# Optimization experiments

Hardware: AMD Instinct MI355X
Metric: run time of the kernel (lower is better)

Reference implementation:

```python
import jax, jax.numpy as jnp
import numpy as np

N, E, D, H, Z, HEADS = 20000, 160000, 3000, 512, 50, 3
EPS = 1e-5


def _bn(x, gamma, beta):
    # BatchNorm1d, training-mode stats (biased variance), eps=1e-5
    m = x.mean(axis=0)
    v = x.var(axis=0)
    return (x - m) * jax.lax.rsqrt(v + EPS) * gamma + beta


def _gat(x, src, dst, n, W, att_src, att_dst, bias, heads, c):
    # PyG GATConv, concat=False (mean over heads), negative_slope=0.2
    h = (x @ W).reshape(n, heads, c)                      # [N,H,C]
    a_s = (h * att_src).sum(-1)                           # [N,H]
    a_d = (h * att_dst).sum(-1)                           # [N,H]
    e = jax.nn.leaky_relu(a_s[src] + a_d[dst], 0.2)       # [Etot,H]
    e = e - jax.ops.segment_max(e, dst, num_segments=n)[dst]
    ex = jnp.exp(e)
    den = jax.ops.segment_sum(ex, dst, num_segments=n)[dst]
    alpha = ex / den                                      # segment softmax over incoming edges
    msg = h[src] * alpha[:, :, None]                      # [Etot,H,C]
    out = jax.ops.segment_sum(msg, dst, num_segments=n)   # [N,H,C]
    return out.mean(axis=1) + bias


def setup_inputs() -> dict:
    key = jax.random.key(0)
    ks = jax.random.split(key, 16)
    s = 0.05
    inp = {
        "x": jax.random.normal(ks[0], (N, D), dtype=jnp.float32),
        "edge_index": jax.random.randint(ks[1], (2, E), 0, N, dtype=jnp.int64),
        "W1": jax.random.normal(ks[2], (D, HEADS * H), dtype=jnp.float32) * s,
        "att_src1": jax.random.normal(ks[3], (HEADS, H), dtype=jnp.float32) * s,
        "att_dst1": jax.random.normal(ks[4], (HEADS, H), dtype=jnp.float32) * s,
        "b1": jnp.zeros((H,), jnp.float32),
        "bn1_g": jnp.ones((H,), jnp.float32),
        "bn1_b": jnp.zeros((H,), jnp.float32),
        "W2": jax.random.normal(ks[5], (H, HEADS * Z), dtype=jnp.float32) * s,
        "att_src2": jax.random.normal(ks[6], (HEADS, Z), dtype=jnp.float32) * s,
        "att_dst2": jax.random.normal(ks[7], (HEADS, Z), dtype=jnp.float32) * s,
        "b2": jnp.zeros((Z,), jnp.float32),
        "bn2_g": jnp.ones((Z,), jnp.float32),
        "bn2_b": jnp.zeros((Z,), jnp.float32),
        "lin1_w": jax.random.normal(ks[8], (H, Z), dtype=jnp.float32) * s,
        "lin1_b": jnp.zeros((H,), jnp.float32),
        "dbn_g": jnp.ones((H,), jnp.float32),
        "dbn_b": jnp.zeros((H,), jnp.float32),
        "lin2_w": jax.random.normal(ks[9], (D, H), dtype=jnp.float32) * s,
        "lin2_b": jnp.zeros((D,), jnp.float32),
    }
    return inp


def reference(x, edge_index, W1, att_src1, att_dst1, b1, bn1_g, bn1_b,
              W2, att_src2, att_dst2, b2, bn2_g, bn2_b,
              lin1_w, lin1_b, dbn_g, dbn_b, lin2_w, lin2_b):
    n = x.shape[0]
    loop = jnp.arange(n, dtype=edge_index.dtype)
    src = jnp.concatenate([edge_index[0], loop])  # add self-loops (PyG default)
    dst = jnp.concatenate([edge_index[1], loop])
    h = jax.nn.relu(_bn(_gat(x, src, dst, n, W1, att_src1, att_dst1, b1, HEADS, H), bn1_g, bn1_b))
    z = jax.nn.relu(_bn(_gat(h, src, dst, n, W2, att_src2, att_dst2, b2, HEADS, Z), bn2_g, bn2_b))
    d = jax.nn.relu(_bn(z @ lin1_w.T + lin1_b, dbn_g, dbn_b))
    out = jax.nn.relu(d @ lin2_w.T + lin2_b)
    return out
```

## Files before the change

### kernel.cpp

```cpp
#include <hip/hip_runtime.h>
#include <stdint.h>

typedef unsigned short u16;
typedef __attribute__((ext_vector_type(8))) short s16x8;
typedef __attribute__((ext_vector_type(4))) short s16x4;
typedef __attribute__((ext_vector_type(4))) float f32x4;

#define DEVFN static __device__ __forceinline__

static constexpr int NN = 20000;
static constexpr int EE = 160000;
static constexpr int ET = 180000;
static constexpr int DD = 3000;
static constexpr int HH = 512;
static constexpr int ZZ = 50;
static constexpr int C1 = 1536;
static constexpr int C2 = 150;
static constexpr int KA1 = 3008;
static constexpr int KP1 = 3072;

DEVFN u16 f2b(float f) {
  uint32_t u = __builtin_bit_cast(uint32_t, f);
  u += 0x7FFFu + ((u >> 16) & 1u);
  return (u16)(u >> 16);
}
DEVFN float b2f(u16 b) {
  uint32_t u = ((uint32_t)b) << 16;
  return __builtin_bit_cast(float, u);
}
DEVFN int edge_at(const void* ei, int mode32, long idx) {
  return mode32 ? ((const int*)ei)[idx] : (int)((const long long*)ei)[idx];
}

typedef __attribute__((address_space(1))) const unsigned int gas_uint;
typedef __attribute__((address_space(3))) unsigned int las_uint;
DEVFN void async16(const u16* g, u16* l) {
  __builtin_amdgcn_global_load_lds((gas_uint*)(uintptr_t)g,
                                   (las_uint*)(unsigned)(uintptr_t)l, 16, 0, 0);
}

__global__ void k_detect(const int* __restrict__ ei, int* __restrict__ mode) {
  __shared__ int nz;
  if (threadIdx.x == 0) nz = 0;
  __syncthreads();
  int loc = 0;
  for (int i = threadIdx.x; i < 1024; i += blockDim.x)
    if (ei[2 * i + 1] != 0) loc = 1;
  if (loc) atomicOr(&nz, 1);
  __syncthreads();
  if (threadIdx.x == 0) *mode = nz;
}

__global__ void k_deg(const void* ei, const int* __restrict__ mode, int* __restrict__ deg) {
  int m = *mode;
  long i = (long)blockIdx.x * blockDim.x + threadIdx.x;
  long st = (long)gridDim.x * blockDim.x;
  for (; i < ET; i += st) {
    int d = (i < EE) ? edge_at(ei, m, EE + i) : (int)(i - EE);
    if ((unsigned)d < (unsigned)NN) atomicAdd(&deg[d], 1);
  }
}

__global__ void k_scan_blk(const int* __restrict__ deg, int* __restrict__ rowptr,
                           int* __restrict__ bsum) {
  __shared__ int buf[256];
  int b = blockIdx.x, tid = threadIdx.x;
  int i = b * 256 + tid;
  buf[tid] = (i < NN) ? deg[i] : 0;
  __syncthreads();
  for (int off = 1; off < 256; off <<= 1) {
    int t = (tid >= off) ? buf[tid - off] : 0;
    __syncthreads();
    buf[tid] += t;
    __syncthreads();
  }
  if (i < NN) rowptr[i + 1] = buf[tid];
  if (tid == 255) bsum[b] = buf[255];
}
__global__ void k_scan_top(int* __restrict__ bsum, int nb) {
  __shared__ int buf[128];
  int tid = threadIdx.x;
  buf[tid] = (tid < nb) ? bsum[tid] : 0;
  __syncthreads();
  for (int off = 1; off < 128; off <<= 1) {
    int t = (tid >= off) ? buf[tid - off] : 0;
    __syncthreads();
    buf[tid] += t;
    __syncthreads();
  }
  if (tid < nb) bsum[tid] = buf[tid];
}
__global__ void k_scan_add(int* __restrict__ rowptr, const int* __restrict__ bsum) {
  int b = blockIdx.x, tid = threadIdx.x;
  int i = b * 256 + tid;
  if (i == 0) rowptr[0] = 0;
  if (b > 0 && i < NN) rowptr[i + 1] += bsum[b - 1];
}

__global__ void k_fill(const void* ei, const int* __restrict__ mode,
                       const int* __restrict__ rowptr, int* __restrict__ cursor,
                       int* __restrict__ srcp) {
  int m = *mode;
  long i = (long)blockIdx.x * blockDim.x + threadIdx.x;
  long st = (long)gridDim.x * blockDim.x;
  for (; i < ET; i += st) {
    int s, d;
    if (i < EE) { s = edge_at(ei, m, i); d = edge_at(ei, m, EE + i); }
    else { s = d = (int)(i - EE); }
    if ((unsigned)d < (unsigned)NN && (unsigned)s < (unsigned)NN) {
      int pos = atomicAdd(&cursor[d], 1);
      srcp[rowptr[d] + pos] = s;
    }
  }
}

__global__ void k_cvt_pad4(const float* __restrict__ in, u16* __restrict__ out,
                           int R, int Cin, int ldo) {
  int r = blockIdx.y;
  int c = (blockIdx.x * blockDim.x + threadIdx.x) * 4;
  if (c >= ldo) return;
  s16x4 o;
  const float* src = in + (size_t)r * Cin + c;
  if (r < R && c + 4 <= Cin && ((((size_t)r * Cin + c) & 3) == 0)) {
    f32x4 v = *(const f32x4*)src;
#pragma unroll
    for (int j = 0; j < 4; j++) o[j] = (short)f2b(v[j]);
  } else {
#pragma unroll
    for (int j = 0; j < 4; j++)
      o[j] = (short)((r < R && c + j < Cin) ? f2b(src[j]) : (u16)0);
  }
  *(s16x4*)(out + (size_t)r * ldo + c) = o;
}

__global__ void k_transpose_tile(const float* __restrict__ in, u16* __restrict__ out,
                                 int R, int Cc, int ldo) {
  __shared__ float t[32][33];
  int tx = threadIdx.x & 31, ty = threadIdx.x >> 5;
  int c0 = blockIdx.x * 32, r0 = blockIdx.y * 32;
#pragma unroll
  for (int j = 0; j < 4; j++) {
    int r = r0 + ty + j * 8, c = c0 + tx;
    t[ty + j * 8][tx] = (r < R && c < Cc) ? in[(size_t)r * Cc + c] : 0.f;
  }
  __syncthreads();
#pragma unroll
  for (int j = 0; j < 4; j++) {
    int c = c0 + ty + j * 8, r = r0 + tx;
    if (c < Cc && r < ldo) out[(size_t)c * ldo + r] = f2b(t[tx][ty + j * 8]);
  }
}

__global__ void k_transpose_cvt2(const float* __restrict__ in, u16* __restrict__ out,
                                 int R, int C, int Cp, int ldo) {
  long total = (long)Cp * ldo;
  long i = (long)blockIdx.x * blockDim.x + threadIdx.x;
  long st = (long)gridDim.x * blockDim.x;
  for (; i < total; i += st) {
    int c = (int)(i / ldo), r = (int)(i % ldo);
    out[i] = (c < C && r < R) ? f2b(in[(size_t)r * C + c]) : (u16)0;
  }
}

template<bool OUT_BF16, bool RELU>
__global__ __launch_bounds__(512, 2) void k_gemm8(
    const u16* __restrict__ Ag, const u16* __restrict__ Bg, void* __restrict__ Cg,
    const float* __restrict__ bias, int M, int Nn, int Kp, int lda, int ldb, int ldc) {
  __shared__ __align__(16) u16 As[2][256][64];
  __shared__ __align__(16) u16 Bs[2][256][64];
  int tid = threadIdx.x;
  int lane = tid & 63, wid = tid >> 6;
  int wm = wid >> 2, wn = wid & 3;
  int lr = lane & 15, lg = lane >> 4;
  int rx = lr & 7;

  int nwg = gridDim.x * gridDim.y;
  int wg = blockIdx.y * gridDim.x + blockIdx.x;
  int q = nwg >> 3, r = nwg & 7;
  int xcd = wg & 7, loc = wg >> 3;
  int swz = (xcd < r ? xcd * (q + 1) : r * (q + 1) + (xcd - r) * q) + loc;
  int m0 = (swz / gridDim.x) * 256, n0 = (swz % gridDim.x) * 256;

  int srow = tid >> 3;
  int schunk = ((tid & 7) ^ (srow & 7)) * 8;
  const u16* agp[4];
  const u16* bgp[4];
#pragma unroll
  for (int i = 0; i < 4; i++) {
    int ra = i * 64 + srow;
    int ga = m0 + ra; if (ga > M - 1) ga = M - 1;
    agp[i] = Ag + (size_t)ga * lda + schunk;
    bgp[i] = Bg + (size_t)(n0 + ra) * ldb + schunk;
  }
  u16* aB0 = &As[0][0][0]; u16* aB1 = &As[1][0][0];
  u16* bB0 = &Bs[0][0][0]; u16* bB1 = &Bs[1][0][0];

#define SA(cb, h, kt) do {                                                  \
    u16* d_ = ((cb) ? aB1 : aB0);                                           \
    async16(agp[2*(h)]   + (size_t)(kt)*64, d_ + (2*(h))*4096 + wid*512);   \
    async16(agp[2*(h)+1] + (size_t)(kt)*64, d_ + (2*(h)+1)*4096 + wid*512); \
  } while (0)
#define SB(cb, h, kt) do {                                                  \
    u16* d_ = ((cb) ? bB1 : bB0);                                           \
    async16(bgp[2*(h)]   + (size_t)(kt)*64, d_ + (2*(h))*4096 + wid*512);   \
    async16(bgp[2*(h)+1] + (size_t)(kt)*64, d_ + (2*(h)+1)*4096 + wid*512); \
  } while (0)
#define BARX() do { asm volatile("" ::: "memory");                          \
    __builtin_amdgcn_s_barrier(); asm volatile("" ::: "memory"); } while (0)
#define VMC4() asm volatile("s_waitcnt vmcnt(4)" ::: "memory")
#define RDA(dst, cb, mi, ks) dst = *(const s16x8*)&As[cb][wm*128+(mi)*16+lr][(((ks)*4+lg)^rx)*8]
#define RDB(dst, cb, ni, ks) dst = *(const s16x8*)&Bs[cb][wn*64+(ni)*16+lr][(((ks)*4+lg)^rx)*8]

  f32x4 acc[8][4];
#pragma unroll
  for (int mi = 0; mi < 8; mi++)
#pragma unroll
    for (int ni = 0; ni < 4; ni++) {
      acc[mi][ni][0] = 0.f; acc[mi][ni][1] = 0.f;
      acc[mi][ni][2] = 0.f; acc[mi][ni][3] = 0.f;
    }

  s16x8 bfr[2][4];
  s16x8 fA0, fA1, fB0, fB1;

#define DO_MFMA(P) do {                                                         \
    _Pragma("unroll")                                                           \
    for (int ni_ = 0; ni_ < 4; ni_++) {                                         \
      acc[2*(P)][ni_]   = __builtin_amdgcn_mfma_f32_16x16x32_bf16(fA0, bfr[0][ni_], acc[2*(P)][ni_], 0, 0, 0);   \
      acc[2*(P)][ni_]   = __builtin_amdgcn_mfma_f32_16x16x32_bf16(fA1, bfr[1][ni_], acc[2*(P)][ni_], 0, 0, 0);   \
      acc[2*(P)+1][ni_] = __builtin_amdgcn_mfma_f32_16x16x32_bf16(fB0, bfr[0][ni_], acc[2*(P)+1][ni_], 0, 0, 0); \
      acc[2*(P)+1][ni_] = __builtin_amdgcn_mfma_f32_16x16x32_bf16(fB1, bfr[1][ni_], acc[2*(P)+1][ni_], 0, 0, 0); \
    } } while (0)

#define PHASE(cb, P, STAGE_STMT, VM_STMT) do {                                  \
    if ((P) == 0) {                                                             \
      RDB(bfr[0][0], cb, 0, 0); RDB(bfr[0][1], cb, 1, 0);                       \
      RDB(bfr[0][2], cb, 2, 0); RDB(bfr[0][3], cb, 3, 0);                       \
      RDB(bfr[1][0], cb, 0, 1); RDB(bfr[1][1], cb, 1, 1);                       \
      RDB(bfr[1][2], cb, 2, 1); RDB(bfr[1][3], cb, 3, 1);                       \
    }                                                                           \
    RDA(fA0, cb, 2*(P), 0);   RDA(fA1, cb, 2*(P), 1);                           \
    RDA(fB0, cb, 2*(P)+1, 0); RDA(fB1, cb, 2*(P)+1, 1);                         \
    STAGE_STMT;                                                                 \
    BARX();                                                                     \
    __builtin_amdgcn_s_setprio(1);                                              \
    DO_MFMA(P);                                                                 \
    __builtin_amdgcn_s_setprio(0);                                              \
    VM_STMT;                                                                    \
    BARX();                                                                     \
  } while (0)

  int nt = Kp >> 6;
  SB(0, 0, 0); SB(0, 1, 0);
  SA(0, 0, 0); SA(0, 1, 0);
  { int k1 = 1 < nt ? 1 : nt - 1; SB(1, 0, k1); SB(1, 1, k1); }
  VMC4();
  BARX();

  for (int t = 0; t < nt; t += 2) {
    int t2 = (t + 2 < nt) ? t + 2 : nt - 1;
    int t3 = (t + 3 < nt) ? t + 3 : nt - 1;
    PHASE(0, 0, SA(1, 0, t + 1), (void)0);
    PHASE(0, 1, SA(1, 1, t + 1), (void)0);
    PHASE(0, 2, SB(0, 0, t2),    (void)0);
    PHASE(0, 3, SB(0, 1, t2),    VMC4());
    PHASE(1, 0, SA(0, 0, t2),    (void)0);
    PHASE(1, 1, SA(0, 1, t2),    (void)0);
    PHASE(1, 2, SB(1, 0, t3),    (void)0);
    PHASE(1, 3, SB(1, 1, t3),    VMC4());
  }
  asm volatile("s_waitcnt vmcnt(0)" ::: "memory");

#undef SA
#undef SB
#undef BARX
#undef VMC4
#undef RDA
#undef RDB
#undef DO_MFMA
#undef PHASE

#pragma unroll
  for (int mi = 0; mi < 8; mi++)
#pragma unroll
    for (int ni = 0; ni < 4; ni++) {
      int col = n0 + wn * 64 + ni * 16 + lr;
      if (col >= Nn) continue;
      float bv = bias ? bias[col] : 0.f;
#pragma unroll
      for (int j = 0; j < 4; j++) {
        int row = m0 + wm * 128 + mi * 16 + lg * 4 + j;
        if (row >= M) continue;
        float v = acc[mi][ni][j] + bv;
        if (RELU) v = v > 0.f ? v : 0.f;
        if (OUT_BF16) ((u16*)Cg)[(size_t)row * ldc + col] = f2b(v);
        else          ((float*)Cg)[(size_t)row * ldc + col] = v;
      }
    }
}

template<bool OUT_BF16, bool RELU>
__global__ __launch_bounds__(256) void k_gemm3(
    const u16* __restrict__ Ag, const u16* __restrict__ Bg, void* __restrict__ Cg,
    const float* __restrict__ bias, int M, int Nn, int Kp, int ld, int ldc) {
  __shared__ __align__(16) u16 As[2][128][64];
  __shared__ __align__(16) u16 Bs[2][128][64];
  int tid = threadIdx.x;
  int lane = tid & 63, wid = tid >> 6;
  int wm = wid >> 1, wn = wid & 1;
  int lr = lane & 15, lg = lane >> 4;

  int nwg = gridDim.x * gridDim.y;
  int wg = blockIdx.y * gridDim.x + blockIdx.x;
  int q = nwg >> 3, r = nwg & 7;
  int xcd = wg & 7, loc = wg >> 3;
  int swz = (xcd < r ? xcd * (q + 1) : r * (q + 1) + (xcd - r) * q) + loc;
  int m0 = (swz / gridDim.x) * 128, n0 = (swz % gridDim.x) * 128;

  int srow = lane >> 3;
  int skk = ((lane & 7) ^ srow) * 8;
  const u16* agp[4];
  const u16* bgp[4];
#pragma unroll
  for (int i = 0; i < 4; i++) {
    int ra = wid * 32 + i * 8 + srow;
    int ga = m0 + ra; if (ga > M - 1) ga = M - 1;
    agp[i] = Ag + (size_t)ga * ld + skk;
    bgp[i] = Bg + (size_t)(n0 + ra) * ld + skk;
  }

#define STAGE(bufi, kofs) do {                                   \
    u16* la_ = &As[bufi][0][0] + wid * 2048;                     \
    u16* lb_ = &Bs[bufi][0][0] + wid * 2048;                     \
    _Pragma("unroll")                                            \
    for (int i_ = 0; i_ < 4; i_++) {                             \
      async16(agp[i_] + (kofs), la_ + i_ * 512);                 \
      async16(bgp[i_] + (kofs), lb_ + i_ * 512);                 \
    }                                                            \
  } while (0)

  f32x4 acc[4][4];
#pragma unroll
  for (int mi = 0; mi < 4; mi++)
#pragma unroll
    for (int ni = 0; ni < 4; ni++) {
      acc[mi][ni][0] = 0.f; acc[mi][ni][1] = 0.f; acc[mi][ni][2] = 0.f; acc[mi][ni][3] = 0.f;
    }

  int rx = lr & 7;
  int NT = Kp >> 6;
  STAGE(0, 0);
  for (int t = 0; t < NT; t++) {
    int cur = t & 1;
    if (t + 1 < NT) {
      STAGE(cur ^ 1, (t + 1) * 64);
      asm volatile("s_waitcnt vmcnt(8)" ::: "memory");
    } else {
      asm volatile("s_waitcnt vmcnt(0)" ::: "memory");
    }
    __builtin_amdgcn_s_barrier();
    asm volatile("" ::: "memory");
#pragma unroll
    for (int ks = 0; ks < 2; ks++) {
      int ch = ((ks * 4 + lg) ^ rx) * 8;
      s16x8 a[4], b[4];
#pragma unroll
      for (int mi = 0; mi < 4; mi++)
        a[mi] = *(const s16x8*)&As[cur][wm * 64 + mi * 16 + lr][ch];
#pragma unroll
      for (int ni = 0; ni < 4; ni++)
        b[ni] = *(const s16x8*)&Bs[cur][wn * 64 + ni * 16 + lr][ch];
#pragma unroll
      for (int mi = 0; mi < 4; mi++)
#pragma unroll
        for (int ni = 0; ni < 4; ni++)
          acc[mi][ni] = __builtin_amdgcn_mfma_f32_16x16x32_bf16(a[mi], b[ni], acc[mi][ni], 0, 0, 0);
    }
    asm volatile("" ::: "memory");
    __builtin_amdgcn_s_barrier();
  }
#undef STAGE

#pragma unroll
  for (int mi = 0; mi < 4; mi++)
#pragma unroll
    for (int ni = 0; ni < 4; ni++) {
      int col = n0 + wn * 64 + ni * 16 + lr;
      if (col >= Nn) continue;
      float bv = bias ? bias[col] : 0.f;
#pragma unroll
      for (int j = 0; j < 4; j++) {
        int row = m0 + wm * 64 + mi * 16 + lg * 4 + j;
        if (row >= M) continue;
        float v = acc[mi][ni][j] + bv;
        if (RELU) v = v > 0.f ? v : 0.f;
        if (OUT_BF16) ((u16*)Cg)[(size_t)row * ldc + col] = f2b(v);
        else          ((float*)Cg)[(size_t)row * ldc + col] = v;
      }
    }
}

__global__ void k_attdot1b(const u16* __restrict__ h1b, const float* __restrict__ asrc,
                           const float* __restrict__ adst, float* __restrict__ as_,
                           float* __restrict__ ad_, float* __restrict__ z0,
                           float* __restrict__ z1) {
  int n = blockIdx.x;
  if (n == 0) {
    for (int i = threadIdx.x; i < HH; i += 192) { z0[i] = 0.f; z1[i] = 0.f; }
  }
  int hd = threadIdx.x >> 6, lane = threadIdx.x & 63;
  s16x8 h = *(const s16x8*)(h1b + (size_t)n * C1 + hd * 512 + lane * 8);
  const float* ap = asrc + hd * 512 + lane * 8;
  const float* dp = adst + hd * 512 + lane * 8;
  f32x4 a0 = *(const f32x4*)ap, a1 = *(const f32x4*)(ap + 4);
  f32x4 d0 = *(const f32x4*)dp, d1 = *(const f32x4*)(dp + 4);
  float ps = 0.f, pd = 0.f;
#pragma unroll
  for (int j = 0; j < 4; j++) {
    float hv = b2f((u16)h[j]);
    ps += hv * a0[j]; pd += hv * d0[j];
    float hw = b2f((u16)h[j + 4]);
    ps += hw * a1[j]; pd += hw * d1[j];
  }
  for (int off = 32; off; off >>= 1) { ps += __shfl_xor(ps, off); pd += __shfl_xor(pd, off); }
  if (lane == 0) { as_[3 * n + hd] = ps; ad_[3 * n + hd] = pd; }
}

__global__ void k_attdot2(const float* __restrict__ s2, const float* __restrict__ asrc,
                          const float* __restrict__ adst, float* __restrict__ as_,
                          float* __restrict__ ad_, float* __restrict__ z0,
                          float* __restrict__ z1, float* __restrict__ z2,
                          float* __restrict__ z3) {
  int n = blockIdx.x, tid = threadIdx.x;
  if (n == 0) {
    for (int i = tid; i < HH; i += 64) { z2[i] = 0.f; z3[i] = 0.f; }
    if (tid < 50) { z0[tid] = 0.f; z1[tid] = 0.f; }
  }
  for (int hd = 0; hd < 3; hd++) {
    float ps = 0.f, pd = 0.f;
    if (tid < 50) {
      float v = s2[(size_t)n * C2 + hd * 50 + tid];
      ps = v * asrc[hd * 50 + tid];
      pd = v * adst[hd * 50 + tid];
    }
    for (int off = 32; off; off >>= 1) { ps += __shfl_xor(ps, off); pd += __shfl_xor(pd, off); }
    if (tid == 0) { as_[3 * n + hd] = ps; ad_[3 * n + hd] = pd; }
  }
}

__global__ __launch_bounds__(192) void k_gat1(
    const u16* __restrict__ h1b, const float* __restrict__ as1,
    const float* __restrict__ ad1, const int* __restrict__ rowptr,
    const int* __restrict__ srcp, const float* __restrict__ bias,
    float* __restrict__ out) {
  int n = blockIdx.x, tid = threadIdx.x;
  __shared__ float sm[3], sden[3];
  __shared__ int s_src[128];
  __shared__ float s_alpha[128][3];
  __shared__ float part[3][512];
  int r0 = rowptr[n], deg = rowptr[n + 1] - r0;
  float adl[3] = {ad1[3 * n], ad1[3 * n + 1], ad1[3 * n + 2]};

  if (tid < 64) {
    float mx[3] = {-1e30f, -1e30f, -1e30f};
    for (int e = tid; e < deg; e += 64) {
      int s = srcp[r0 + e];
#pragma unroll
      for (int hd = 0; hd < 3; hd++) {
        float v = as1[3 * s + hd] + adl[hd];
        v = v > 0.f ? v : 0.2f * v;
        mx[hd] = fmaxf(mx[hd], v);
      }
    }
#pragma unroll
    for (int hd = 0; hd < 3; hd++)
      for (int off = 32; off; off >>= 1) mx[hd] = fmaxf(mx[hd], __shfl_xor(mx[hd], off));
    float sd[3] = {0.f, 0.f, 0.f};
    for (int e = tid; e < deg; e += 64) {
      int s = srcp[r0 + e];
#pragma unroll
      for (int hd = 0; hd < 3; hd++) {
        float v = as1[3 * s + hd] + adl[hd];
        v = v > 0.f ? v : 0.2f * v;
        sd[hd] += __expf(v - mx[hd]);
      }
    }
#pragma unroll
    for (int hd = 0; hd < 3; hd++)
      for (int off = 32; off; off >>= 1) sd[hd] += __shfl_xor(sd[hd], off);
    if (tid == 0) {
#pragma unroll
      for (int hd = 0; hd < 3; hd++) { sm[hd] = mx[hd]; sden[hd] = sd[hd]; }
    }
  }
  __syncthreads();

  int hd = tid >> 6, lane = tid & 63;
  float a[8];
#pragma unroll
  for (int j = 0; j < 8; j++) a[j] = 0.f;

  for (int base = 0; base < deg; base += 128) {
    int cnt = min(128, deg - base);
    if (tid < cnt) {
      int s = srcp[r0 + base + tid];
      s_src[tid] = s;
#pragma unroll
      for (int h2 = 0; h2 < 3; h2++) {
        float v = as1[3 * s + h2] + adl[h2];
        v = v > 0.f ? v : 0.2f * v;
        s_alpha[tid][h2] = __expf(v - sm[h2]) / sden[h2];
      }
    }
    __syncthreads();
    int e = 0;
    for (; e + 2 <= cnt; e += 2) {
      const u16* p0 = h1b + (size_t)s_src[e] * C1 + (hd << 9) + lane * 8;
      const u16* p1 = h1b + (size_t)s_src[e + 1] * C1 + (hd << 9) + lane * 8;
      s16x8 v0 = *(const s16x8*)p0;
      s16x8 v1 = *(const s16x8*)p1;
      float al0 = s_alpha[e][hd], al1 = s_alpha[e + 1][hd];
#pragma unroll
      for (int j = 0; j < 8; j++)
        a[j] += al0 * b2f((u16)v0[j]) + al1 * b2f((u16)v1[j]);
    }
    if (e < cnt) {
      const u16* p0 = h1b + (size_t)s_src[e] * C1 + (hd << 9) + lane * 8;
      s16x8 v0 = *(const s16x8*)p0;
      float al0 = s_alpha[e][hd];
#pragma unroll
      for (int j = 0; j < 8; j++) a[j] += al0 * b2f((u16)v0[j]);
    }
    __syncthreads();
  }

#pragma unroll
  for (int j = 0; j < 8; j++) part[hd][lane * 8 + j] = a[j];
  __syncthreads();
  if (tid < 128) {
    f32x4 p0 = *(const f32x4*)&part[0][tid * 4];
    f32x4 p1 = *(const f32x4*)&part[1][tid * 4];
    f32x4 p2 = *(const f32x4*)&part[2][tid * 4];
    f32x4 bv = *(const f32x4*)(bias + tid * 4);
    f32x4 o;
#pragma unroll
    for (int j = 0; j < 4; j++) o[j] = (p0[j] + p1[j] + p2[j]) * (1.f / 3.f) + bv[j];
    *(f32x4*)(out + (size_t)n * 512 + tid * 4) = o;
  }
}

__global__ void k_gat2(const float* __restrict__ s2, const float* __restrict__ as2,
                       const float* __restrict__ ad2, const int* __restrict__ rowptr,
                       const int* __restrict__ srcp, const float* __restrict__ bias,
                       float* __restrict__ z) {
  int n = blockIdx.x, tid = threadIdx.x;
  __shared__ int s_src[64];
  __shared__ float s_alpha[64][3];
  int r0 = rowptr[n], deg = rowptr[n + 1] - r0;
  float adl[3] = {ad2[3 * n], ad2[3 * n + 1], ad2[3 * n + 2]};

  float mx[3] = {-1e30f, -1e30f, -1e30f};
  for (int e = tid; e < deg; e += 64) {
    int s = srcp[r0 + e];
#pragma unroll
    for (int hd = 0; hd < 3; hd++) {
      float v = as2[3 * s + hd] + adl[hd];
      v = v > 0.f ? v : 0.2f * v;
      mx[hd] = fmaxf(mx[hd], v);
    }
  }
#pragma unroll
  for (int hd = 0; hd < 3; hd++)
    for (int off = 32; off; off >>= 1) mx[hd] = fmaxf(mx[hd], __shfl_xor(mx[hd], off));
  float sd[3] = {0.f, 0.f, 0.f};
  for (int e = tid; e < deg; e += 64) {
    int s = srcp[r0 + e];
#pragma unroll
    for (int hd = 0; hd < 3; hd++) {
      float v = as2[3 * s + hd] + adl[hd];
      v = v > 0.f ? v : 0.2f * v;
      sd[hd] += __expf(v - mx[hd]);
    }
  }
#pragma unroll
  for (int hd = 0; hd < 3; hd++)
    for (int off = 32; off; off >>= 1) sd[hd] += __shfl_xor(sd[hd], off);

  float acc = 0.f;
  for (int base = 0; base < deg; base += 64) {
    int cnt = min(64, deg - base);
    if (tid < cnt) {
      int s = srcp[r0 + base + tid];
      s_src[tid] = s;
#pragma unroll
      for (int hd = 0; hd < 3; hd++) {
        float v = as2[3 * s + hd] + adl[hd];
        v = v > 0.f ? v : 0.2f * v;
        s_alpha[tid][hd] = __expf(v - mx[hd]) / sd[hd];
      }
    }
    __syncthreads();
    if (tid < 50) {
      for (int e = 0; e < cnt; e++) {
        const float* row = s2 + (size_t)s_src[e] * C2;
#pragma unroll
        for (int hd = 0; hd < 3; hd++) acc += s_alpha[e][hd] * row[hd * 50 + tid];
      }
    }
    __syncthreads();
  }
  if (tid < 50) z[(size_t)n * ZZ + tid] = acc * (1.f / 3.f) + bias[tid];
}

__global__ void k_colstats3(const float* __restrict__ x, float* __restrict__ gsum,
                            float* __restrict__ gsq, long total, int C) {
  long i = (long)blockIdx.x * blockDim.x + threadIdx.x;
  long st = (long)gridDim.x * blockDim.x;
  int c = (int)(i % C);
  float s = 0.f, q = 0.f;
  for (; i < total; i += st) { float v = x[i]; s += v; q += v * v; }
  atomicAdd(&gsum[c], s);
  atomicAdd(&gsq[c], q);
}

__global__ void k_bnfinal(const float* __restrict__ gsum, const float* __restrict__ gsq,
                          const float* __restrict__ g, const float* __restrict__ b,
                          float* __restrict__ scale, float* __restrict__ shift,
                          int C, float invN) {
  int c = blockIdx.x * blockDim.x + threadIdx.x;
  if (c < C) {
    float m = gsum[c] * invN;
    float var = gsq[c] * invN - m * m;
    float rs = rsqrtf(var + 1e-5f);
    float sc = g[c] * rs;
    scale[c] = sc;
    shift[c] = b[c] - m * sc;
  }
}

__global__ void k_bnrelu4(const float* __restrict__ x, const float* __restrict__ sc,
                          const float* __restrict__ sh, u16* __restrict__ out, long total4) {
  long i = (long)blockIdx.x * blockDim.x + threadIdx.x;
  long st = (long)gridDim.x * blockDim.x;
  for (; i < total4; i += st) {
    long b = i * 4;
    int c = (int)(b & 511);
    f32x4 v = *(const f32x4*)(x + b);
    f32x4 s = *(const f32x4*)(sc + c);
    f32x4 t = *(const f32x4*)(sh + c);
    s16x4 o;
#pragma unroll
    for (int j = 0; j < 4; j++) {
      float r = v[j] * s[j] + t[j];
      r = r > 0.f ? r : 0.f;
      o[j] = (short)f2b(r);
    }
    *(s16x4*)(out + b) = o;
  }
}

__global__ void k_bnrelu_pad(const float* __restrict__ x, const float* __restrict__ sc,
                             const float* __restrict__ sh, u16* __restrict__ out) {
  int i = blockIdx.x * blockDim.x + threadIdx.x;
  if (i >= NN * 64) return;
  int c = i & 63, r = i >> 6;
  float v = 0.f;
  if (c < 50) {
    v = x[r * 50 + c] * sc[c] + sh[c];
    v = v > 0.f ? v : 0.f;
  }
  out[i] = f2b(v);
}

extern "C" void kernel_launch(void* const* d_in, const int* in_sizes, int n_in,
                              void* d_out, int out_size, void* d_ws, size_t ws_size,
                              hipStream_t stream) {
  (void)in_sizes; (void)n_in; (void)out_size;
  const float* x     = (const float*)d_in[0];
  const void*  ei    = d_in[1];
  const float* W1    = (const float*)d_in[2];
  const float* asrc1 = (const float*)d_in[3];
  const float* adst1 = (const float*)d_in[4];
  const float* b1    = (const float*)d_in[5];
  const float* bn1g  = (const float*)d_in[6];
  const float* bn1b  = (const float*)d_in[7];
  const float* W2    = (const float*)d_in[8];
  const float* asrc2 = (const float*)d_in[9];
  const float* adst2 = (const float*)d_in[10];
  const float* b2    = (const float*)d_in[11];
  const float* bn2g  = (const float*)d_in[12];
  const float* bn2b  = (const float*)d_in[13];
  const float* l1w   = (const float*)d_in[14];
  const float* l1b   = (const float*)d_in[15];
  const float* dbng  = (const float*)d_in[16];
  const float* dbnb  = (const float*)d_in[17];
  const float* l2w   = (const float*)d_in[18];
  const float* l2b   = (const float*)d_in[19];
  float* out = (float*)d_out;
  char* ws = (char*)d_ws;

  size_t off = 0;
  auto alloc = [&](size_t b) { size_t r = off; off += (b + 255) & ~(size_t)255; return r; };
  const size_t oXB  = alloc(120320000);
  const size_t oH1  = alloc(61440000);
  const size_t oW1T = alloc((size_t)C1 * KP1 * 2);
  const size_t oAS1 = alloc((size_t)NN * 12), oAD1 = alloc((size_t)NN * 12);
  const size_t oAS2 = alloc((size_t)NN * 12), oAD2 = alloc((size_t)NN * 12);
  const size_t oRP  = alloc((size_t)(NN + 1) * 4);
  const size_t oDEG = alloc((size_t)NN * 4);
  const size_t oSRC = alloc((size_t)ET * 4);
  const size_t oMODE = alloc(256);
  const size_t oBSUM = alloc(512);
  const size_t oS1 = alloc(2048), oQ1 = alloc(2048);
  const size_t oS2 = alloc(2048), oQ2 = alloc(2048);
  const size_t oS3 = alloc(2048), oQ3 = alloc(2048);
  const size_t oSC = alloc(2048), oSH = alloc(2048);
  if (ws_size < off) return;

  u16*   xb   = (u16*)(ws + oXB);
  float* g1   = (float*)(ws + oXB);
  u16*   h2b  = (u16*)(ws + oXB + 40960000);
  float* s2   = (float*)(ws + oXB + 61440000);
  float* zf   = (float*)(ws + oXB + 73440000);
  u16*   zb   = (u16*)(ws + oXB + 77440000);
  u16*   w2T  = (u16*)(ws + oXB + 80000000);
  u16*   l1wT = (u16*)(ws + oXB + 80262400);
  u16*   l2wT = (u16*)(ws + oXB + 80328192);
  float* dbuf = (float*)(ws + oXB);
  u16*   h1b  = (u16*)(ws + oH1);
  u16*   db   = (u16*)(ws + oH1);
  u16*   w1T  = (u16*)(ws + oW1T);
  int* mode   = (int*)(ws + oMODE);
  int* bsum   = (int*)(ws + oBSUM);
  int* deg    = (int*)(ws + oDEG);
  int* rowptr = (int*)(ws + oRP);
  int* srcp   = (int*)(ws + oSRC);
  float *as1 = (float*)(ws + oAS1), *ad1 = (float*)(ws + oAD1);
  float *as2 = (float*)(ws + oAS2), *ad2 = (float*)(ws + oAD2);
  float *sum1 = (float*)(ws + oS1), *sq1 = (float*)(ws + oQ1);
  float *sum2 = (float*)(ws + oS2), *sq2 = (float*)(ws + oQ2);
  float *sum3 = (float*)(ws + oS3), *sq3 = (float*)(ws + oQ3);
  float *bsc = (float*)(ws + oSC), *bsh = (float*)(ws + oSH);

  k_detect<<<1, 256, 0, stream>>>((const int*)ei, mode);
  hipMemsetAsync(deg, 0, (size_t)NN * 4, stream);
  k_deg<<<512, 256, 0, stream>>>(ei, mode, deg);
  k_scan_blk<<<79, 256, 0, stream>>>(deg, rowptr, bsum);
  k_scan_top<<<1, 128, 0, stream>>>(bsum, 79);
  k_scan_add<<<79, 256, 0, stream>>>(rowptr, bsum);
  hipMemsetAsync(deg, 0, (size_t)NN * 4, stream);
  k_fill<<<512, 256, 0, stream>>>(ei, mode, rowptr, deg, srcp);

  k_cvt_pad4<<<dim3(3, NN), 256, 0, stream>>>(x, xb, NN, DD, KA1);
  k_transpose_tile<<<dim3(C1 / 32, KP1 / 32), 256, 0, stream>>>(W1, w1T, DD, C1, KP1);
  k_gemm8<true, false><<<dim3(6, 79), 512, 0, stream>>>(xb, w1T, h1b, nullptr,
                                                        NN, C1, KP1, KA1, KP1, C1);
  k_attdot1b<<<NN, 192, 0, stream>>>(h1b, asrc1, adst1, as1, ad1, sum1, sq1);
  k_gat1<<<NN, 192, 0, stream>>>(h1b, as1, ad1, rowptr, srcp, b1, g1);
  k_colstats3<<<512, 256, 0, stream>>>(g1, sum1, sq1, (long)NN * HH, HH);
  k_bnfinal<<<2, 256, 0, stream>>>(sum1, sq1, bn1g, bn1b, bsc, bsh, HH, 1.0f / NN);
  k_bnrelu4<<<2048, 256, 0, stream>>>(g1, bsc, bsh, h2b, (long)NN * HH / 4);

  k_transpose_cvt2<<<256, 256, 0, stream>>>(W2, w2T, HH, C2, 256, HH);
  k_gemm3<false, false><<<dim3(2, 157), 256, 0, stream>>>(h2b, w2T, s2, nullptr,
                                                          NN, C2, HH, HH, C2);
  k_attdot2<<<NN, 64, 0, stream>>>(s2, asrc2, adst2, as2, ad2, sum2, sq2, sum3, sq3);
  k_gat2<<<NN, 64, 0, stream>>>(s2, as2, ad2, rowptr, srcp, b2, zf);
  k_colstats3<<<25, 256, 0, stream>>>(zf, sum2, sq2, (long)NN * ZZ, ZZ);
  k_bnfinal<<<1, 64, 0, stream>>>(sum2, sq2, bn2g, bn2b, bsc, bsh, ZZ, 1.0f / NN);
  k_bnrelu_pad<<<5000, 256, 0, stream>>>(zf, bsc, bsh, zb);

  k_cvt_pad4<<<dim3(1, HH), 256, 0, stream>>>(l1w, l1wT, HH, ZZ, 64);
  k_gemm3<false, false><<<dim3(4, 157), 256, 0, stream>>>(zb, l1wT, dbuf, l1b,
                                                          NN, HH, 64, 64, HH);
  k_colstats3<<<512, 256, 0, stream>>>(dbuf, sum3, sq3, (long)NN * HH, HH);
  k_bnfinal<<<2, 256, 0, stream>>>(sum3, sq3, dbng, dbnb, bsc, bsh, HH, 1.0f / NN);
  k_bnrelu4<<<2048, 256, 0, stream>>>(dbuf, bsc, bsh, db, (long)NN * HH / 4);
  k_cvt_pad4<<<dim3(1, 3072), 256, 0, stream>>>(l2w, l2wT, DD, HH, HH);
  k_gemm8<false, true><<<dim3(12, 79), 512, 0, stream>>>(db, l2wT, out, l2b,
                                                         NN, DD, 512, HH, HH, DD);
}
```

Before: 724.3 us.

## Cut launches by fusing BN finalize and mode detection, software-pipeline GEMM LDS reads

Removes the k_detect, k_bnfinal launches and one memset by folding edge-dtype detection into k_deg/k_fill, recomputing BN scale/shift inside the BN+ReLU kernels, and zeroing the degree array inside the scan kernel. The gemm8 main loop is restructured so the LDS fragment reads for the next phase are issued alongside the MFMAs of the current phase, using two fragment register sets to hide LDS latency. In exchange, every BN element recomputes an rsqrt, each block re-reads the detection sample, and register pressure in the GEMM rises.

```diff
diff --git a/kernel.cpp b/kernel.cpp
--- a/kernel.cpp
+++ b/kernel.cpp
@@ -39,20 +39,21 @@
                                    (las_uint*)(unsigned)(uintptr_t)l, 16, 0, 0);
 }
 
-__global__ void k_detect(const int* __restrict__ ei, int* __restrict__ mode) {
-  __shared__ int nz;
-  if (threadIdx.x == 0) nz = 0;
+DEVFN int sniff_mode(const void* ei, int* nzsh) {
+  if (threadIdx.x == 0) *nzsh = 0;
   __syncthreads();
+  const int* e32 = (const int*)ei;
   int loc = 0;
   for (int i = threadIdx.x; i < 1024; i += blockDim.x)
-    if (ei[2 * i + 1] != 0) loc = 1;
-  if (loc) atomicOr(&nz, 1);
+    if (e32[2 * i + 1] != 0) loc = 1;
+  if (loc) atomicOr(nzsh, 1);
   __syncthreads();
-  if (threadIdx.x == 0) *mode = nz;
-}
-
-__global__ void k_deg(const void* ei, const int* __restrict__ mode, int* __restrict__ deg) {
-  int m = *mode;
+  return *nzsh;
+}
+
+__global__ void k_deg(const void* ei, int* __restrict__ deg) {
+  __shared__ int nz;
+  int m = sniff_mode(ei, &nz);
   long i = (long)blockIdx.x * blockDim.x + threadIdx.x;
   long st = (long)gridDim.x * blockDim.x;
   for (; i < ET; i += st) {
@@ -61,12 +62,13 @@
   }
 }
 
-__global__ void k_scan_blk(const int* __restrict__ deg, int* __restrict__ rowptr,
+__global__ void k_scan_blk(int* __restrict__ deg, int* __restrict__ rowptr,
                            int* __restrict__ bsum) {
   __shared__ int buf[256];
   int b = blockIdx.x, tid = threadIdx.x;
   int i = b * 256 + tid;
   buf[tid] = (i < NN) ? deg[i] : 0;
+  if (i < NN) deg[i] = 0;
   __syncthreads();
   for (int off = 1; off < 256; off <<= 1) {
     int t = (tid >= off) ? buf[tid - off] : 0;
@@ -97,10 +99,10 @@
   if (b > 0 && i < NN) rowptr[i + 1] += bsum[b - 1];
 }
 
-__global__ void k_fill(const void* ei, const int* __restrict__ mode,
-                       const int* __restrict__ rowptr, int* __restrict__ cursor,
-                       int* __restrict__ srcp) {
-  int m = *mode;
+__global__ void k_fill(const void* ei, const int* __restrict__ rowptr,
+                       int* __restrict__ cursor, int* __restrict__ srcp) {
+  __shared__ int nz;
+  int m = sniff_mode(ei, &nz);
   long i = (long)blockIdx.x * blockDim.x + threadIdx.x;
   long st = (long)gridDim.x * blockDim.x;
   for (; i < ET; i += st) {
@@ -221,33 +223,43 @@
     }
 
   s16x8 bfr[2][4];
-  s16x8 fA0, fA1, fB0, fB1;
-
-#define DO_MFMA(P) do {                                                         \
-    _Pragma("unroll")                                                           \
-    for (int ni_ = 0; ni_ < 4; ni_++) {                                         \
-      acc[2*(P)][ni_]   = __builtin_amdgcn_mfma_f32_16x16x32_bf16(fA0, bfr[0][ni_], acc[2*(P)][ni_], 0, 0, 0);   \
-      acc[2*(P)][ni_]   = __builtin_amdgcn_mfma_f32_16x16x32_bf16(fA1, bfr[1][ni_], acc[2*(P)][ni_], 0, 0, 0);   \
-      acc[2*(P)+1][ni_] = __builtin_amdgcn_mfma_f32_16x16x32_bf16(fB0, bfr[0][ni_], acc[2*(P)+1][ni_], 0, 0, 0); \
-      acc[2*(P)+1][ni_] = __builtin_amdgcn_mfma_f32_16x16x32_bf16(fB1, bfr[1][ni_], acc[2*(P)+1][ni_], 0, 0, 0); \
+  s16x8 f0[4], f1[4];
+
+#define RDB8(cb) do {                                                   \
+    RDB(bfr[0][0], cb, 0, 0); RDB(bfr[0][1], cb, 1, 0);                 \
+    RDB(bfr[0][2], cb, 2, 0); RDB(bfr[0][3], cb, 3, 0);                 \
+    RDB(bfr[1][0], cb, 0, 1); RDB(bfr[1][1], cb, 1, 1);                 \
+    RDB(bfr[1][2], cb, 2, 1); RDB(bfr[1][3], cb, 3, 1); } while (0)
+#define RDAP(F, cb, P) do {                                             \
+    RDA(F[0], cb, 2*(P), 0);   RDA(F[1], cb, 2*(P), 1);                 \
+    RDA(F[2], cb, 2*(P)+1, 0); RDA(F[3], cb, 2*(P)+1, 1); } while (0)
+#define DO_MFMA(P, F) do {                                              \
+    _Pragma("unroll")                                                   \
+    for (int ni_ = 0; ni_ < 4; ni_++) {                                 \
+      acc[2*(P)][ni_]   = __builtin_amdgcn_mfma_f32_16x16x32_bf16(F[0], bfr[0][ni_], acc[2*(P)][ni_], 0, 0, 0);   \
+      acc[2*(P)][ni_]   = __builtin_amdgcn_mfma_f32_16x16x32_bf16(F[1], bfr[1][ni_], acc[2*(P)][ni_], 0, 0, 0);   \
+      acc[2*(P)+1][ni_] = __builtin_amdgcn_mfma_f32_16x16x32_bf16(F[2], bfr[0][ni_], acc[2*(P)+1][ni_], 0, 0, 0); \
+      acc[2*(P)+1][ni_] = __builtin_amdgcn_mfma_f32_16x16x32_bf16(F[3], bfr[1][ni_], acc[2*(P)+1][ni_], 0, 0, 0); \
     } } while (0)
 
-#define PHASE(cb, P, STAGE_STMT, VM_STMT) do {                                  \
-    if ((P) == 0) {                                                             \
-      RDB(bfr[0][0], cb, 0, 0); RDB(bfr[0][1], cb, 1, 0);                       \
-      RDB(bfr[0][2], cb, 2, 0); RDB(bfr[0][3], cb, 3, 0);                       \
-      RDB(bfr[1][0], cb, 0, 1); RDB(bfr[1][1], cb, 1, 1);                       \
-      RDB(bfr[1][2], cb, 2, 1); RDB(bfr[1][3], cb, 3, 1);                       \
-    }                                                                           \
-    RDA(fA0, cb, 2*(P), 0);   RDA(fA1, cb, 2*(P), 1);                           \
-    RDA(fB0, cb, 2*(P)+1, 0); RDA(fB1, cb, 2*(P)+1, 1);                         \
-    STAGE_STMT;                                                                 \
-    BARX();                                                                     \
-    __builtin_amdgcn_s_setprio(1);                                              \
-    DO_MFMA(P);                                                                 \
-    __builtin_amdgcn_s_setprio(0);                                              \
-    VM_STMT;                                                                    \
-    BARX();                                                                     \
+#define GROUP(cb, S1, S2, S3, S4) do {                                  \
+    RDB8(cb); RDAP(f0, cb, 0);                                          \
+    S1; BARX();                                                         \
+    __builtin_amdgcn_s_setprio(1);                                      \
+    RDAP(f1, cb, 1); DO_MFMA(0, f0);                                    \
+    __builtin_amdgcn_s_setprio(0); BARX();                              \
+    S2; BARX();                                                         \
+    __builtin_amdgcn_s_setprio(1);                                      \
+    RDAP(f0, cb, 2); DO_MFMA(1, f1);                                    \
+    __builtin_amdgcn_s_setprio(0); BARX();                              \
+    S3; BARX();                                                         \
+    __builtin_amdgcn_s_setprio(1);                                      \
+    RDAP(f1, cb, 3); DO_MFMA(2, f0);                                    \
+    __builtin_amdgcn_s_setprio(0); BARX();                              \
+    S4; BARX();                                                         \
+    __builtin_amdgcn_s_setprio(1);                                      \
+    DO_MFMA(3, f1);                                                     \
+    __builtin_amdgcn_s_setprio(0); VMC4(); BARX();                      \
   } while (0)
 
   int nt = Kp >> 6;
@@ -260,14 +272,8 @@
   for (int t = 0; t < nt; t += 2) {
     int t2 = (t + 2 < nt) ? t + 2 : nt - 1;
     int t3 = (t + 3 < nt) ? t + 3 : nt - 1;
-    PHASE(0, 0, SA(1, 0, t + 1), (void)0);
-    PHASE(0, 1, SA(1, 1, t + 1), (void)0);
-    PHASE(0, 2, SB(0, 0, t2),    (void)0);
-    PHASE(0, 3, SB(0, 1, t2),    VMC4());
-    PHASE(1, 0, SA(0, 0, t2),    (void)0);
-    PHASE(1, 1, SA(0, 1, t2),    (void)0);
-    PHASE(1, 2, SB(1, 0, t3),    (void)0);
-    PHASE(1, 3, SB(1, 1, t3),    VMC4());
+    GROUP(0, SA(1, 0, t + 1), SA(1, 1, t + 1), SB(0, 0, t2), SB(0, 1, t2));
+    GROUP(1, SA(0, 0, t2),    SA(0, 1, t2),    SB(1, 0, t3), SB(1, 1, t3));
   }
   asm volatile("s_waitcnt vmcnt(0)" ::: "memory");
 
@@ -277,8 +283,10 @@
 #undef VMC4
 #undef RDA
 #undef RDB
+#undef RDB8
+#undef RDAP
 #undef DO_MFMA
-#undef PHASE
+#undef GROUP
 
 #pragma unroll
   for (int mi = 0; mi < 8; mi++)
@@ -623,35 +631,27 @@
   atomicAdd(&gsq[c], q);
 }
 
-__global__ void k_bnfinal(const float* __restrict__ gsum, const float* __restrict__ gsq,
-                          const float* __restrict__ g, const float* __restrict__ b,
-                          float* __restrict__ scale, float* __restrict__ shift,
-                          int C, float invN) {
-  int c = blockIdx.x * blockDim.x + threadIdx.x;
-  if (c < C) {
-    float m = gsum[c] * invN;
-    float var = gsq[c] * invN - m * m;
-    float rs = rsqrtf(var + 1e-5f);
-    float sc = g[c] * rs;
-    scale[c] = sc;
-    shift[c] = b[c] - m * sc;
-  }
-}
-
-__global__ void k_bnrelu4(const float* __restrict__ x, const float* __restrict__ sc,
-                          const float* __restrict__ sh, u16* __restrict__ out, long total4) {
+__global__ void k_bnrelu4f(const float* __restrict__ x, const float* __restrict__ gsum,
+                           const float* __restrict__ gsq, const float* __restrict__ g,
+                           const float* __restrict__ bb, u16* __restrict__ out,
+                           long total4, float invN) {
   long i = (long)blockIdx.x * blockDim.x + threadIdx.x;
   long st = (long)gridDim.x * blockDim.x;
   for (; i < total4; i += st) {
     long b = i * 4;
     int c = (int)(b & 511);
     f32x4 v = *(const f32x4*)(x + b);
-    f32x4 s = *(const f32x4*)(sc + c);
-    f32x4 t = *(const f32x4*)(sh + c);
+    f32x4 s = *(const f32x4*)(gsum + c);
+    f32x4 qv = *(const f32x4*)(gsq + c);
+    f32x4 gg = *(const f32x4*)(g + c);
+    f32x4 bv = *(const f32x4*)(bb + c);
     s16x4 o;
 #pragma unroll
     for (int j = 0; j < 4; j++) {
-      float r = v[j] * s[j] + t[j];
+      float m = s[j] * invN;
+      float var = qv[j] * invN - m * m;
+      float sc = gg[j] * rsqrtf(var + 1e-5f);
+      float r = (v[j] - m) * sc + bv[j];
       r = r > 0.f ? r : 0.f;
       o[j] = (short)f2b(r);
     }
@@ -659,14 +659,18 @@
   }
 }
 
-__global__ void k_bnrelu_pad(const float* __restrict__ x, const float* __restrict__ sc,
-                             const float* __restrict__ sh, u16* __restrict__ out) {
+__global__ void k_bnrelu_padf(const float* __restrict__ x, const float* __restrict__ gsum,
+                              const float* __restrict__ gsq, const float* __restrict__ g,
+                              const float* __restrict__ bb, u16* __restrict__ out) {
   int i = blockIdx.x * blockDim.x + threadIdx.x;
   if (i >= NN * 64) return;
   int c = i & 63, r = i >> 6;
   float v = 0.f;
   if (c < 50) {
-    v = x[r * 50 + c] * sc[c] + sh[c];
+    float m = gsum[c] * (1.0f / NN);
+    float var = gsq[c] * (1.0f / NN) - m * m;
+    float sc = g[c] * rsqrtf(var + 1e-5f);
+    v = (x[r * 50 + c] - m) * sc + bb[c];
     v = v > 0.f ? v : 0.f;
   }
   out[i] = f2b(v);
@@ -709,12 +713,10 @@
   const size_t oRP  = alloc((size_t)(NN + 1) * 4);
   const size_t oDEG = alloc((size_t)NN * 4);
   const size_t oSRC = alloc((size_t)ET * 4);
-  const size_t oMODE = alloc(256);
   const size_t oBSUM = alloc(512);
   const size_t oS1 = alloc(2048), oQ1 = alloc(2048);
   const size_t oS2 = alloc(2048), oQ2 = alloc(2048);
   const size_t oS3 = alloc(2048), oQ3 = alloc(2048);
-  const size_t oSC = alloc(2048), oSH = alloc(2048);
   if (ws_size < off) return;
 
   u16*   xb   = (u16*)(ws + oXB);
@@ -730,7 +732,6 @@
   u16*   h1b  = (u16*)(ws + oH1);
   u16*   db   = (u16*)(ws + oH1);
   u16*   w1T  = (u16*)(ws + oW1T);
-  int* mode   = (int*)(ws + oMODE);
   int* bsum   = (int*)(ws + oBSUM);
   int* deg    = (int*)(ws + oDEG);
   int* rowptr = (int*)(ws + oRP);
@@ -740,16 +741,13 @@
   float *sum1 = (float*)(ws + oS1), *sq1 = (float*)(ws + oQ1);
   float *sum2 = (float*)(ws + oS2), *sq2 = (float*)(ws + oQ2);
   float *sum3 = (float*)(ws + oS3), *sq3 = (float*)(ws + oQ3);
-  float *bsc = (float*)(ws + oSC), *bsh = (float*)(ws + oSH);
-
-  k_detect<<<1, 256, 0, stream>>>((const int*)ei, mode);
+
   hipMemsetAsync(deg, 0, (size_t)NN * 4, stream);
-  k_deg<<<512, 256, 0, stream>>>(ei, mode, deg);
+  k_deg<<<512, 256, 0, stream>>>(ei, deg);
   k_scan_blk<<<79, 256, 0, stream>>>(deg, rowptr, bsum);
   k_scan_top<<<1, 128, 0, stream>>>(bsum, 79);
   k_scan_add<<<79, 256, 0, stream>>>(rowptr, bsum);
-  hipMemsetAsync(deg, 0, (size_t)NN * 4, stream);
-  k_fill<<<512, 256, 0, stream>>>(ei, mode, rowptr, deg, srcp);
+  k_fill<<<512, 256, 0, stream>>>(ei, rowptr, deg, srcp);
 
   k_cvt_pad4<<<dim3(3, NN), 256, 0, stream>>>(x, xb, NN, DD, KA1);
   k_transpose_tile<<<dim3(C1 / 32, KP1 / 32), 256, 0, stream>>>(W1, w1T, DD, C1, KP1);
@@ -758,8 +756,8 @@
   k_attdot1b<<<NN, 192, 0, stream>>>(h1b, asrc1, adst1, as1, ad1, sum1, sq1);
   k_gat1<<<NN, 192, 0, stream>>>(h1b, as1, ad1, rowptr, srcp, b1, g1);
   k_colstats3<<<512, 256, 0, stream>>>(g1, sum1, sq1, (long)NN * HH, HH);
-  k_bnfinal<<<2, 256, 0, stream>>>(sum1, sq1, bn1g, bn1b, bsc, bsh, HH, 1.0f / NN);
-  k_bnrelu4<<<2048, 256, 0, stream>>>(g1, bsc, bsh, h2b, (long)NN * HH / 4);
+  k_bnrelu4f<<<2048, 256, 0, stream>>>(g1, sum1, sq1, bn1g, bn1b, h2b,
+                                       (long)NN * HH / 4, 1.0f / NN);
 
   k_transpose_cvt2<<<256, 256, 0, stream>>>(W2, w2T, HH, C2, 256, HH);
   k_gemm3<false, false><<<dim3(2, 157), 256, 0, stream>>>(h2b, w2T, s2, nullptr,
@@ -767,15 +765,14 @@
   k_attdot2<<<NN, 64, 0, stream>>>(s2, asrc2, adst2, as2, ad2, sum2, sq2, sum3, sq3);
   k_gat2<<<NN, 64, 0, stream>>>(s2, as2, ad2, rowptr, srcp, b2, zf);
   k_colstats3<<<25, 256, 0, stream>>>(zf, sum2, sq2, (long)NN * ZZ, ZZ);
-  k_bnfinal<<<1, 64, 0, stream>>>(sum2, sq2, bn2g, bn2b, bsc, bsh, ZZ, 1.0f / NN);
-  k_bnrelu_pad<<<5000, 256, 0, stream>>>(zf, bsc, bsh, zb);
+  k_bnrelu_padf<<<5000, 256, 0, stream>>>(zf, sum2, sq2, bn2g, bn2b, zb);
 
   k_cvt_pad4<<<dim3(1, HH), 256, 0, stream>>>(l1w, l1wT, HH, ZZ, 64);
   k_gemm3<false, false><<<dim3(4, 157), 256, 0, stream>>>(zb, l1wT, dbuf, l1b,
                                                           NN, HH, 64, 64, HH);
   k_colstats3<<<512, 256, 0, stream>>>(dbuf, sum3, sq3, (long)NN * HH, HH);
-  k_bnfinal<<<2, 256, 0, stream>>>(sum3, sq3, dbng, dbnb, bsc, bsh, HH, 1.0f / NN);
-  k_bnrelu4<<<2048, 256, 0, stream>>>(dbuf, bsc, bsh, db, (long)NN * HH / 4);
+  k_bnrelu4f<<<2048, 256, 0, stream>>>(dbuf, sum3, sq3, dbng, dbnb, db,
+                                       (long)NN * HH / 4, 1.0f / NN);
   k_cvt_pad4<<<dim3(1, 3072), 256, 0, stream>>>(l2w, l2wT, DD, HH, HH);
   k_gemm8<false, true><<<dim3(12, 79), 512, 0, stream>>>(db, l2wT, out, l2b,
                                                          NN, DD, 512, HH, HH, DD);
```

Result: no change. 718.8 us (-0.8%).
